# Performance work log

Measured on AMD Instinct MI355X. Metric: run time of the kernel, lower is better.

Reference implementation:

```python
import jax, jax.numpy as jnp
import numpy as np

N_EMBED = 512  # c in the original; scale uses sqrt(c), not head_size


def setup_inputs() -> dict:
    key = jax.random.key(0)
    k1, k2, k3, k4 = jax.random.split(key, 4)
    B, T, C, H = 4, 4096, N_EMBED, 64
    x = jax.random.normal(k1, (B, T, C), dtype=jnp.float32)
    Wk = jax.random.normal(k2, (C, H), dtype=jnp.float32) * (1.0 / np.sqrt(C))
    Wq = jax.random.normal(k3, (C, H), dtype=jnp.float32) * (1.0 / np.sqrt(C))
    Wv = jax.random.normal(k4, (C, H), dtype=jnp.float32) * (1.0 / np.sqrt(C))
    return {"x": x, "Wk": Wk, "Wq": Wq, "Wv": Wv}


def reference(x, Wk, Wq, Wv):
    # x: [B, T, C]; Wk/Wq/Wv: [C, H]
    B, T, C = x.shape
    k = jnp.einsum('btc,ch->bth', x, Wk)
    q = jnp.einsum('btc,ch->bth', x, Wq)
    v = jnp.einsum('btc,ch->bth', x, Wv)
    scale = 1.0 / jnp.sqrt(jnp.float32(C))  # original divides by sqrt(c)
    scores = jnp.einsum('bth,bsh->bts', q, k) * scale  # [B, T, T]
    causal = jnp.tril(jnp.ones((T, T), dtype=bool))
    scores = jnp.where(causal, scores, -jnp.inf)
    attn = jax.nn.softmax(scores, axis=-1)
    # dropout = 0.0 -> identity
    out = jnp.einsum('bts,bsh->bth', attn, v)  # [B, T, H]
    return out
```

## Files before the change

kernel.cpp:

```cpp
#include <hip/hip_runtime.h>
#include <hip/hip_bf16.h>
#include <math.h>

#define NB 4
#define NT 4096
#define NC 512
#define NH 64
#define QBLK 64
#define KVBLK 64
#define LDK 72
#define MASKV (-1e30f)

typedef __attribute__((ext_vector_type(8))) short bf16x8;
typedef __attribute__((ext_vector_type(4))) float f32x4;

__device__ inline unsigned short f2bf(float f) {
    __hip_bfloat16 h = __float2bfloat16(f);
    return *reinterpret_cast<unsigned short*>(&h);
}

__device__ inline int part_slot(int b, int qt, int ch) {
    int m = qt >> 3, r = qt & 7;
    return b * 288 + qt + 4 * m * (m - 1) + r * m + ch;
}

__global__ __launch_bounds__(256) void wconv(
    const float* __restrict__ Wk, const float* __restrict__ Wq,
    const float* __restrict__ Wv, unsigned short* __restrict__ Wt)
{
    int idx = blockIdx.x * 256 + threadIdx.x;
    int n = idx % 192, c = idx / 192;
    int sel = n >> 6, h = n & 63;
    const float* W = (sel == 0) ? Wq : (sel == 1) ? Wk : Wv;
    float val = W[c * NH + h];
    if (sel == 0) val *= 0.044194173824159216f;
    Wt[n * NC + c] = f2bf(val);
}

__global__ __launch_bounds__(256) void qkv_gemm(
    const float* __restrict__ x, const unsigned short* __restrict__ Wt,
    unsigned short* __restrict__ q, unsigned short* __restrict__ k,
    unsigned short* __restrict__ v)
{
    __shared__ unsigned short xa[32][LDK];
    __shared__ unsigned short wb[192][LDK];

    const int tid = threadIdx.x;
    const int w = tid >> 6, lane = tid & 63, l15 = lane & 15, g = lane >> 4;
    const size_t r0 = (size_t)blockIdx.x * 32;

    f32x4 acc[2][3];
    #pragma unroll
    for (int mt = 0; mt < 2; ++mt)
        #pragma unroll
        for (int nt = 0; nt < 3; ++nt) acc[mt][nt] = (f32x4){0.f,0.f,0.f,0.f};

    for (int c0 = 0; c0 < NC; c0 += 64) {
        __syncthreads();
        {
            int row = tid >> 3, f8 = tid & 7;
            const float* xp = x + (r0 + row) * NC + c0 + f8*8;
            float4 x0 = *reinterpret_cast<const float4*>(xp);
            float4 x1 = *reinterpret_cast<const float4*>(xp + 4);
            bf16x8 a8;
            a8[0]=f2bf(x0.x); a8[1]=f2bf(x0.y); a8[2]=f2bf(x0.z); a8[3]=f2bf(x0.w);
            a8[4]=f2bf(x1.x); a8[5]=f2bf(x1.y); a8[6]=f2bf(x1.z); a8[7]=f2bf(x1.w);
            *reinterpret_cast<bf16x8*>(&xa[row][f8*8]) = a8;
        }
        #pragma unroll
        for (int i = 0; i < 6; ++i) {
            int idx = tid + 256*i;
            int row = idx >> 3, f8 = idx & 7;
            bf16x8 w8 = *reinterpret_cast<const bf16x8*>(Wt + (size_t)row * NC + c0 + f8*8);
            *reinterpret_cast<bf16x8*>(&wb[row][f8*8]) = w8;
        }
        __syncthreads();

        #pragma unroll
        for (int kk = 0; kk < 2; ++kk) {
            bf16x8 a[2], bfr[3];
            #pragma unroll
            for (int mt = 0; mt < 2; ++mt)
                a[mt] = *reinterpret_cast<const bf16x8*>(&xa[16*mt + l15][32*kk + 8*g]);
            #pragma unroll
            for (int nt = 0; nt < 3; ++nt)
                bfr[nt] = *reinterpret_cast<const bf16x8*>(&wb[48*w + 16*nt + l15][32*kk + 8*g]);
            __builtin_amdgcn_s_setprio(1);
            #pragma unroll
            for (int mt = 0; mt < 2; ++mt)
                #pragma unroll
                for (int nt = 0; nt < 3; ++nt)
                    acc[mt][nt] = __builtin_amdgcn_mfma_f32_16x16x32_bf16(a[mt], bfr[nt], acc[mt][nt], 0, 0, 0);
            __builtin_amdgcn_s_setprio(0);
        }
    }

    #pragma unroll
    for (int mt = 0; mt < 2; ++mt)
        #pragma unroll
        for (int nt = 0; nt < 3; ++nt) {
            int ncol = 48*w + 16*nt + l15;
            int sel = ncol >> 6, h = ncol & 63;
            unsigned short* dst = (sel == 0) ? q : (sel == 1) ? k : v;
            #pragma unroll
            for (int r = 0; r < 4; ++r)
                dst[(r0 + 16*mt + 4*g + r) * NH + h] = f2bf(acc[mt][nt][r]);
        }
}

__global__ __launch_bounds__(256) void attn_part(
    const unsigned short* __restrict__ qg,
    const unsigned short* __restrict__ kg,
    const unsigned short* __restrict__ vg,
    float* __restrict__ out,
    float* __restrict__ O_part,
    float* __restrict__ ML_part)
{
    const int qt = 63 - blockIdx.x;
    const int ch = blockIdx.y;
    if (8*ch > qt) return;
    const int b  = blockIdx.z;
    const int nch = (qt >> 3) + 1;

    __shared__ unsigned short k_lds[2][KVBLK][LDK];
    __shared__ unsigned short vt_lds[2][NH][LDK];
    __shared__ unsigned short p_lds[4][16][LDK];

    const int tid  = threadIdx.x;
    const int w    = tid >> 6;
    const int lane = tid & 63;
    const int l15  = lane & 15;
    const int g    = lane >> 4;

    const int q0 = qt * QBLK;
    const size_t base = (size_t)b * NT * NH;
    const int qrow  = q0 + 16*w + l15;
    const int wrow0 = q0 + 16*w;
    const int qhi   = wrow0 + 15;

    bf16x8 qf0, qf1;
    {
        const unsigned short* qp = qg + base + (size_t)qrow * NH + 8*g;
        qf0 = *reinterpret_cast<const bf16x8*>(qp);
        qf1 = *reinterpret_cast<const bf16x8*>(qp + 32);
    }

    f32x4 ot[4];
    #pragma unroll
    for (int i = 0; i < 4; ++i) ot[i] = (f32x4){0.f,0.f,0.f,0.f};
    float m = MASKV, lsum = 0.f;

    const int tBeg = 8 * ch;
    const int tEnd = min(8 * (ch + 1), qt + 1);

    const int krow = tid >> 3, kc8 = tid & 7;
    const int vd = lane, vkq = w;

    bf16x8 kpre0, kpre1;
    unsigned short vpre[16];

    {
        const int s0 = tBeg * KVBLK;
        const unsigned short* kp = kg + base + (size_t)(s0 + krow) * NH + kc8*8;
        kpre0 = *reinterpret_cast<const bf16x8*>(kp);
        kpre1 = *reinterpret_cast<const bf16x8*>(kp + 32 * NH);
        #pragma unroll
        for (int i = 0; i < 16; ++i)
            vpre[i] = vg[base + (size_t)(s0 + vkq*16 + i) * NH + vd];
    }

    int cur = 0;
    for (int it = tBeg; it < tEnd; ++it) {
        const int s0 = it * KVBLK;
        *reinterpret_cast<bf16x8*>(&k_lds[cur][krow][kc8*8])      = kpre0;
        *reinterpret_cast<bf16x8*>(&k_lds[cur][krow+32][kc8*8])   = kpre1;
        *reinterpret_cast<bf16x8*>(&vt_lds[cur][vd][vkq*16])      = *reinterpret_cast<bf16x8*>(&vpre[0]);
        *reinterpret_cast<bf16x8*>(&vt_lds[cur][vd][vkq*16 + 8])  = *reinterpret_cast<bf16x8*>(&vpre[8]);
        __syncthreads();

        if (it + 1 < tEnd) {
            const int sn = s0 + KVBLK;
            const unsigned short* kp = kg + base + (size_t)(sn + krow) * NH + kc8*8;
            kpre0 = *reinterpret_cast<const bf16x8*>(kp);
            kpre1 = *reinterpret_cast<const bf16x8*>(kp + 32 * NH);
            #pragma unroll
            for (int i = 0; i < 16; ++i)
                vpre[i] = vg[base + (size_t)(sn + vkq*16 + i) * NH + vd];
        }

        if (s0 <= qhi) {
            f32x4 s[4];
            __builtin_amdgcn_s_setprio(1);
            #pragma unroll
            for (int t = 0; t < 4; ++t) {
                bf16x8 ka = *reinterpret_cast<const bf16x8*>(&k_lds[cur][16*t + l15][8*g]);
                bf16x8 kb = *reinterpret_cast<const bf16x8*>(&k_lds[cur][16*t + l15][8*g + 32]);
                s[t] = __builtin_amdgcn_mfma_f32_16x16x32_bf16(ka, qf0, (f32x4){0.f,0.f,0.f,0.f}, 0, 0, 0);
                s[t] = __builtin_amdgcn_mfma_f32_16x16x32_bf16(kb, qf1, s[t], 0, 0, 0);
            }
            __builtin_amdgcn_s_setprio(0);

            if (s0 + 63 > wrow0) {
                const int kvb = s0 + 4*g;
                #pragma unroll
                for (int t = 0; t < 4; ++t)
                    #pragma unroll
                    for (int r = 0; r < 4; ++r)
                        if (kvb + 16*t + r > qrow) s[t][r] = MASKV;
            }

            float pm = MASKV;
            #pragma unroll
            for (int t = 0; t < 4; ++t)
                #pragma unroll
                for (int r = 0; r < 4; ++r) pm = fmaxf(pm, s[t][r]);
            pm = fmaxf(pm, __shfl_xor(pm, 16));
            pm = fmaxf(pm, __shfl_xor(pm, 32));

            if (!__all(pm <= m + 8.f)) {
                float mn   = fmaxf(m, pm);
                float corr = __expf(m - mn);
                lsum *= corr;
                #pragma unroll
                for (int dt = 0; dt < 4; ++dt)
                    #pragma unroll
                    for (int e = 0; e < 4; ++e) ot[dt][e] *= corr;
                m = mn;
            }

            float ps = 0.f;
            #pragma unroll
            for (int t = 0; t < 4; ++t)
                #pragma unroll
                for (int r = 0; r < 4; ++r) {
                    float pv = __expf(s[t][r] - m);
                    s[t][r] = pv;
                    ps += pv;
                }

            #pragma unroll
            for (int t = 0; t < 4; ++t) {
                unsigned int w0 = (unsigned int)f2bf(s[t][0]) | ((unsigned int)f2bf(s[t][1]) << 16);
                unsigned int w1 = (unsigned int)f2bf(s[t][2]) | ((unsigned int)f2bf(s[t][3]) << 16);
                *reinterpret_cast<unsigned int*>(&p_lds[w][l15][16*t + 4*g])     = w0;
                *reinterpret_cast<unsigned int*>(&p_lds[w][l15][16*t + 4*g + 2]) = w1;
            }

            ps += __shfl_xor(ps, 16);
            ps += __shfl_xor(ps, 32);
            lsum += ps;

            __builtin_amdgcn_s_setprio(1);
            #pragma unroll
            for (int kk = 0; kk < 2; ++kk) {
                bf16x8 pf = *reinterpret_cast<const bf16x8*>(&p_lds[w][l15][8*g + 32*kk]);
                #pragma unroll
                for (int dt = 0; dt < 4; ++dt) {
                    bf16x8 vf = *reinterpret_cast<const bf16x8*>(&vt_lds[cur][16*dt + l15][8*g + 32*kk]);
                    ot[dt] = __builtin_amdgcn_mfma_f32_16x16x32_bf16(vf, pf, ot[dt], 0, 0, 0);
                }
            }
            __builtin_amdgcn_s_setprio(0);
        }
        cur ^= 1;
    }

    if (nch == 1) {
        const float inv = 1.f / lsum;
        float* orow = out + base + (size_t)qrow * NH;
        #pragma unroll
        for (int dt = 0; dt < 4; ++dt) {
            f32x4 o4;
            #pragma unroll
            for (int r = 0; r < 4; ++r) o4[r] = ot[dt][r] * inv;
            *reinterpret_cast<f32x4*>(&orow[16*dt + 4*g]) = o4;
        }
    } else {
        const int slot = part_slot(b, qt, ch);
        float* op = O_part + (size_t)slot * (QBLK*NH) + (size_t)(16*w + l15) * NH;
        #pragma unroll
        for (int dt = 0; dt < 4; ++dt)
            *reinterpret_cast<f32x4*>(&op[16*dt + 4*g]) = ot[dt];
        if (g == 0) {
            float2 ml = make_float2(m, lsum);
            *reinterpret_cast<float2*>(&ML_part[(size_t)slot * 128 + 2*(16*w + l15)]) = ml;
        }
    }
}

__global__ __launch_bounds__(256) void attn_merge(
    const float* __restrict__ O_part,
    const float* __restrict__ ML_part,
    float* __restrict__ out)
{
    const int qt = 8 + blockIdx.x;
    const int b  = blockIdx.y;
    const int nch = (qt >> 3) + 1;
    const int slot0 = part_slot(b, qt, 0);
    const int row = threadIdx.x >> 2;
    const int dq  = (threadIdx.x & 3) * 16;

    float M = MASKV;
    #pragma unroll 2
    for (int c = 0; c < nch; ++c)
        M = fmaxf(M, ML_part[(size_t)(slot0 + c) * 128 + 2*row]);

    float L = 0.f;
    float acc[16];
    #pragma unroll
    for (int j = 0; j < 16; ++j) acc[j] = 0.f;

    for (int c = 0; c < nch; ++c) {
        const float* mlp = &ML_part[(size_t)(slot0 + c) * 128 + 2*row];
        float mc = mlp[0], lc = mlp[1];
        float wgt = __expf(mc - M);
        L += wgt * lc;
        const float* op = O_part + (size_t)(slot0 + c) * (QBLK*NH) + (size_t)row * NH + dq;
        #pragma unroll
        for (int j4 = 0; j4 < 4; ++j4) {
            float4 o4 = *reinterpret_cast<const float4*>(op + 4*j4);
            acc[4*j4+0] = fmaf(wgt, o4.x, acc[4*j4+0]);
            acc[4*j4+1] = fmaf(wgt, o4.y, acc[4*j4+1]);
            acc[4*j4+2] = fmaf(wgt, o4.z, acc[4*j4+2]);
            acc[4*j4+3] = fmaf(wgt, o4.w, acc[4*j4+3]);
        }
    }

    const float inv = 1.f / L;
    float* orow = out + (size_t)b * NT * NH + (size_t)(qt * QBLK + row) * NH + dq;
    #pragma unroll
    for (int j4 = 0; j4 < 4; ++j4) {
        float4 o4;
        o4.x = acc[4*j4+0] * inv;
        o4.y = acc[4*j4+1] * inv;
        o4.z = acc[4*j4+2] * inv;
        o4.w = acc[4*j4+3] * inv;
        *reinterpret_cast<float4*>(orow + 4*j4) = o4;
    }
}

extern "C" void kernel_launch(void* const* d_in, const int* in_sizes, int n_in,
                              void* d_out, int out_size, void* d_ws, size_t ws_size,
                              hipStream_t stream) {
    const float* x  = (const float*)d_in[0];
    const float* Wk = (const float*)d_in[1];
    const float* Wq = (const float*)d_in[2];
    const float* Wv = (const float*)d_in[3];
    float* out = (float*)d_out;

    const size_t n = (size_t)NB * NT * NH;
    unsigned short* qb = (unsigned short*)d_ws;
    unsigned short* kb = qb + n;
    unsigned short* vb = kb + n;
    unsigned short* Wt = vb + n;
    float* O_part  = (float*)(Wt + 192 * NC);
    float* ML_part = O_part + (size_t)1152 * QBLK * NH;

    wconv<<<(192*NC)/256, 256, 0, stream>>>(Wk, Wq, Wv, Wt);
    qkv_gemm<<<(NB*NT)/32, 256, 0, stream>>>(x, Wt, qb, kb, vb);

    dim3 pgrid(64, 8, NB);
    attn_part<<<pgrid, 256, 0, stream>>>(qb, kb, vb, out, O_part, ML_part);
    dim3 mgrid(56, NB);
    attn_merge<<<mgrid, 256, 0, stream>>>(O_part, ML_part, out);
}
```

Baseline: 64.94 us.

## Restructure attention into single-wave 32-row blocks reading K and transposed V directly

The QKV GEMM now writes V already transposed to [B,H,T], so the attention kernel can load V fragments straight from global memory. The attention kernel becomes a one-wave block handling 32 query rows (two 16-row MFMA tiles) with no K/V staging in shared memory and no block barriers, which raises the block count and removes sync and LDS traffic. The split-KV partition and merge indexing are redone for 32-row tiles. The cost is more global/L2 reads, since each wave fetches its own K/V tiles, and a larger partial-result buffer.

```diff
diff --git a/kernel.cpp b/kernel.cpp
--- a/kernel.cpp
+++ b/kernel.cpp
@@ -6,7 +6,6 @@
 #define NT 4096
 #define NC 512
 #define NH 64
-#define QBLK 64
 #define KVBLK 64
 #define LDK 72
 #define MASKV (-1e30f)
@@ -17,11 +16,6 @@
 __device__ inline unsigned short f2bf(float f) {
     __hip_bfloat16 h = __float2bfloat16(f);
     return *reinterpret_cast<unsigned short*>(&h);
-}
-
-__device__ inline int part_slot(int b, int qt, int ch) {
-    int m = qt >> 3, r = qt & 7;
-    return b * 288 + qt + 4 * m * (m - 1) + r * m + ch;
 }
 
 __global__ __launch_bounds__(256) void wconv(
@@ -40,7 +34,7 @@
 __global__ __launch_bounds__(256) void qkv_gemm(
     const float* __restrict__ x, const unsigned short* __restrict__ Wt,
     unsigned short* __restrict__ q, unsigned short* __restrict__ k,
-    unsigned short* __restrict__ v)
+    unsigned short* __restrict__ vt)
 {
     __shared__ unsigned short xa[32][LDK];
     __shared__ unsigned short wb[192][LDK];
@@ -101,189 +95,197 @@
         for (int nt = 0; nt < 3; ++nt) {
             int ncol = 48*w + 16*nt + l15;
             int sel = ncol >> 6, h = ncol & 63;
-            unsigned short* dst = (sel == 0) ? q : (sel == 1) ? k : v;
-            #pragma unroll
-            for (int r = 0; r < 4; ++r)
-                dst[(r0 + 16*mt + 4*g + r) * NH + h] = f2bf(acc[mt][nt][r]);
-        }
-}
-
-__global__ __launch_bounds__(256) void attn_part(
+            if (sel < 2) {
+                unsigned short* dst = (sel == 0) ? q : k;
+                #pragma unroll
+                for (int r = 0; r < 4; ++r)
+                    dst[(r0 + 16*mt + 4*g + r) * NH + h] = f2bf(acc[mt][nt][r]);
+            } else {
+                int bb = (int)(r0 >> 12);
+                int trow = ((int)r0 & (NT-1)) + 16*mt + 4*g;
+                unsigned int lo = (unsigned int)f2bf(acc[mt][nt][0]) | ((unsigned int)f2bf(acc[mt][nt][1]) << 16);
+                unsigned int hi = (unsigned int)f2bf(acc[mt][nt][2]) | ((unsigned int)f2bf(acc[mt][nt][3]) << 16);
+                *reinterpret_cast<uint2*>(&vt[((size_t)bb*NH + h)*NT + trow]) = make_uint2(lo, hi);
+            }
+        }
+}
+
+__global__ __launch_bounds__(64, 3) void attn_part(
     const unsigned short* __restrict__ qg,
     const unsigned short* __restrict__ kg,
-    const unsigned short* __restrict__ vg,
+    const unsigned short* __restrict__ vtg,
     float* __restrict__ out,
     float* __restrict__ O_part,
     float* __restrict__ ML_part)
 {
-    const int qt = 63 - blockIdx.x;
+    const int qt = 127 - blockIdx.x;
+    const int nT = (qt >> 1) + 1;
     const int ch = blockIdx.y;
-    if (8*ch > qt) return;
+    if (8 * ch >= nT) return;
     const int b  = blockIdx.z;
-    const int nch = (qt >> 3) + 1;
-
-    __shared__ unsigned short k_lds[2][KVBLK][LDK];
-    __shared__ unsigned short vt_lds[2][NH][LDK];
-    __shared__ unsigned short p_lds[4][16][LDK];
-
-    const int tid  = threadIdx.x;
-    const int w    = tid >> 6;
-    const int lane = tid & 63;
+
+    __shared__ unsigned short p_lds[32][LDK];
+
+    const int lane = threadIdx.x & 63;
     const int l15  = lane & 15;
     const int g    = lane >> 4;
 
-    const int q0 = qt * QBLK;
+    const int q0 = qt * 32;
     const size_t base = (size_t)b * NT * NH;
-    const int qrow  = q0 + 16*w + l15;
-    const int wrow0 = q0 + 16*w;
-    const int qhi   = wrow0 + 15;
-
-    bf16x8 qf0, qf1;
-    {
-        const unsigned short* qp = qg + base + (size_t)qrow * NH + 8*g;
-        qf0 = *reinterpret_cast<const bf16x8*>(qp);
-        qf1 = *reinterpret_cast<const bf16x8*>(qp + 32);
-    }
-
-    f32x4 ot[4];
-    #pragma unroll
-    for (int i = 0; i < 4; ++i) ot[i] = (f32x4){0.f,0.f,0.f,0.f};
-    float m = MASKV, lsum = 0.f;
+
+    bf16x8 qf[2][2];
+    #pragma unroll
+    for (int qc = 0; qc < 2; ++qc) {
+        const unsigned short* qp = qg + base + (size_t)(q0 + 16*qc + l15) * NH + 8*g;
+        qf[qc][0] = *reinterpret_cast<const bf16x8*>(qp);
+        qf[qc][1] = *reinterpret_cast<const bf16x8*>(qp + 32);
+    }
+
+    f32x4 ot[4][2];
+    #pragma unroll
+    for (int dt = 0; dt < 4; ++dt)
+        #pragma unroll
+        for (int qc = 0; qc < 2; ++qc) ot[dt][qc] = (f32x4){0.f,0.f,0.f,0.f};
+    float m0 = MASKV, m1 = MASKV, l0 = 0.f, l1 = 0.f;
 
     const int tBeg = 8 * ch;
-    const int tEnd = min(8 * (ch + 1), qt + 1);
-
-    const int krow = tid >> 3, kc8 = tid & 7;
-    const int vd = lane, vkq = w;
-
-    bf16x8 kpre0, kpre1;
-    unsigned short vpre[16];
-
-    {
-        const int s0 = tBeg * KVBLK;
-        const unsigned short* kp = kg + base + (size_t)(s0 + krow) * NH + kc8*8;
-        kpre0 = *reinterpret_cast<const bf16x8*>(kp);
-        kpre1 = *reinterpret_cast<const bf16x8*>(kp + 32 * NH);
-        #pragma unroll
-        for (int i = 0; i < 16; ++i)
-            vpre[i] = vg[base + (size_t)(s0 + vkq*16 + i) * NH + vd];
-    }
-
-    int cur = 0;
+    const int tEnd = min(8 * (ch + 1), nT);
+
     for (int it = tBeg; it < tEnd; ++it) {
         const int s0 = it * KVBLK;
-        *reinterpret_cast<bf16x8*>(&k_lds[cur][krow][kc8*8])      = kpre0;
-        *reinterpret_cast<bf16x8*>(&k_lds[cur][krow+32][kc8*8])   = kpre1;
-        *reinterpret_cast<bf16x8*>(&vt_lds[cur][vd][vkq*16])      = *reinterpret_cast<bf16x8*>(&vpre[0]);
-        *reinterpret_cast<bf16x8*>(&vt_lds[cur][vd][vkq*16 + 8])  = *reinterpret_cast<bf16x8*>(&vpre[8]);
-        __syncthreads();
-
-        if (it + 1 < tEnd) {
-            const int sn = s0 + KVBLK;
-            const unsigned short* kp = kg + base + (size_t)(sn + krow) * NH + kc8*8;
-            kpre0 = *reinterpret_cast<const bf16x8*>(kp);
-            kpre1 = *reinterpret_cast<const bf16x8*>(kp + 32 * NH);
-            #pragma unroll
-            for (int i = 0; i < 16; ++i)
-                vpre[i] = vg[base + (size_t)(sn + vkq*16 + i) * NH + vd];
-        }
-
-        if (s0 <= qhi) {
-            f32x4 s[4];
-            __builtin_amdgcn_s_setprio(1);
-            #pragma unroll
-            for (int t = 0; t < 4; ++t) {
-                bf16x8 ka = *reinterpret_cast<const bf16x8*>(&k_lds[cur][16*t + l15][8*g]);
-                bf16x8 kb = *reinterpret_cast<const bf16x8*>(&k_lds[cur][16*t + l15][8*g + 32]);
-                s[t] = __builtin_amdgcn_mfma_f32_16x16x32_bf16(ka, qf0, (f32x4){0.f,0.f,0.f,0.f}, 0, 0, 0);
-                s[t] = __builtin_amdgcn_mfma_f32_16x16x32_bf16(kb, qf1, s[t], 0, 0, 0);
-            }
-            __builtin_amdgcn_s_setprio(0);
-
-            if (s0 + 63 > wrow0) {
-                const int kvb = s0 + 4*g;
-                #pragma unroll
-                for (int t = 0; t < 4; ++t)
+
+        const unsigned short* kbase = kg + base + (size_t)(s0 + l15) * NH + 8*g;
+        bf16x8 ka[4][2];
+        #pragma unroll
+        for (int t = 0; t < 4; ++t)
+            #pragma unroll
+            for (int kk = 0; kk < 2; ++kk)
+                ka[t][kk] = *reinterpret_cast<const bf16x8*>(kbase + t*16*NH + kk*32);
+
+        f32x4 s[4][2];
+        __builtin_amdgcn_s_setprio(1);
+        #pragma unroll
+        for (int t = 0; t < 4; ++t)
+            #pragma unroll
+            for (int qc = 0; qc < 2; ++qc) {
+                s[t][qc] = __builtin_amdgcn_mfma_f32_16x16x32_bf16(ka[t][0], qf[qc][0], (f32x4){0.f,0.f,0.f,0.f}, 0, 0, 0);
+                s[t][qc] = __builtin_amdgcn_mfma_f32_16x16x32_bf16(ka[t][1], qf[qc][1], s[t][qc], 0, 0, 0);
+            }
+        __builtin_amdgcn_s_setprio(0);
+
+        const unsigned short* vbase = vtg + ((size_t)b*NH + l15)*NT + s0 + 8*g;
+        bf16x8 vf[4][2];
+        #pragma unroll
+        for (int dt = 0; dt < 4; ++dt)
+            #pragma unroll
+            for (int kk = 0; kk < 2; ++kk)
+                vf[dt][kk] = *reinterpret_cast<const bf16x8*>(vbase + (size_t)dt*16*NT + kk*32);
+
+        if (s0 + KVBLK - 1 > q0) {
+            #pragma unroll
+            for (int t = 0; t < 4; ++t)
+                #pragma unroll
+                for (int qc = 0; qc < 2; ++qc) {
+                    const int qr = q0 + 16*qc + l15;
                     #pragma unroll
                     for (int r = 0; r < 4; ++r)
-                        if (kvb + 16*t + r > qrow) s[t][r] = MASKV;
-            }
-
-            float pm = MASKV;
-            #pragma unroll
-            for (int t = 0; t < 4; ++t)
-                #pragma unroll
-                for (int r = 0; r < 4; ++r) pm = fmaxf(pm, s[t][r]);
-            pm = fmaxf(pm, __shfl_xor(pm, 16));
-            pm = fmaxf(pm, __shfl_xor(pm, 32));
-
-            if (!__all(pm <= m + 8.f)) {
-                float mn   = fmaxf(m, pm);
-                float corr = __expf(m - mn);
-                lsum *= corr;
-                #pragma unroll
-                for (int dt = 0; dt < 4; ++dt)
-                    #pragma unroll
-                    for (int e = 0; e < 4; ++e) ot[dt][e] *= corr;
-                m = mn;
-            }
-
-            float ps = 0.f;
-            #pragma unroll
-            for (int t = 0; t < 4; ++t)
-                #pragma unroll
-                for (int r = 0; r < 4; ++r) {
-                    float pv = __expf(s[t][r] - m);
-                    s[t][r] = pv;
-                    ps += pv;
+                        if (s0 + 16*t + 4*g + r > qr) s[t][qc][r] = MASKV;
                 }
-
+        }
+
+        float pm0 = MASKV, pm1 = MASKV;
+        #pragma unroll
+        for (int t = 0; t < 4; ++t)
+            #pragma unroll
+            for (int r = 0; r < 4; ++r) {
+                pm0 = fmaxf(pm0, s[t][0][r]);
+                pm1 = fmaxf(pm1, s[t][1][r]);
+            }
+        pm0 = fmaxf(pm0, __shfl_xor(pm0, 16)); pm0 = fmaxf(pm0, __shfl_xor(pm0, 32));
+        pm1 = fmaxf(pm1, __shfl_xor(pm1, 16)); pm1 = fmaxf(pm1, __shfl_xor(pm1, 32));
+
+        if (!__all(pm0 <= m0 + 8.f && pm1 <= m1 + 8.f)) {
+            float mn0 = fmaxf(m0, pm0), mn1 = fmaxf(m1, pm1);
+            float c0 = __expf(m0 - mn0), c1 = __expf(m1 - mn1);
+            l0 *= c0; l1 *= c1;
+            #pragma unroll
+            for (int dt = 0; dt < 4; ++dt)
+                #pragma unroll
+                for (int e = 0; e < 4; ++e) {
+                    ot[dt][0][e] *= c0;
+                    ot[dt][1][e] *= c1;
+                }
+            m0 = mn0; m1 = mn1;
+        }
+
+        float ps0 = 0.f, ps1 = 0.f;
+        #pragma unroll
+        for (int t = 0; t < 4; ++t)
+            #pragma unroll
+            for (int r = 0; r < 4; ++r) {
+                float p0 = __expf(s[t][0][r] - m0);
+                float p1 = __expf(s[t][1][r] - m1);
+                s[t][0][r] = p0; s[t][1][r] = p1;
+                ps0 += p0; ps1 += p1;
+            }
+
+        #pragma unroll
+        for (int qc = 0; qc < 2; ++qc)
             #pragma unroll
             for (int t = 0; t < 4; ++t) {
-                unsigned int w0 = (unsigned int)f2bf(s[t][0]) | ((unsigned int)f2bf(s[t][1]) << 16);
-                unsigned int w1 = (unsigned int)f2bf(s[t][2]) | ((unsigned int)f2bf(s[t][3]) << 16);
-                *reinterpret_cast<unsigned int*>(&p_lds[w][l15][16*t + 4*g])     = w0;
-                *reinterpret_cast<unsigned int*>(&p_lds[w][l15][16*t + 4*g + 2]) = w1;
-            }
-
-            ps += __shfl_xor(ps, 16);
-            ps += __shfl_xor(ps, 32);
-            lsum += ps;
-
-            __builtin_amdgcn_s_setprio(1);
-            #pragma unroll
-            for (int kk = 0; kk < 2; ++kk) {
-                bf16x8 pf = *reinterpret_cast<const bf16x8*>(&p_lds[w][l15][8*g + 32*kk]);
-                #pragma unroll
-                for (int dt = 0; dt < 4; ++dt) {
-                    bf16x8 vf = *reinterpret_cast<const bf16x8*>(&vt_lds[cur][16*dt + l15][8*g + 32*kk]);
-                    ot[dt] = __builtin_amdgcn_mfma_f32_16x16x32_bf16(vf, pf, ot[dt], 0, 0, 0);
-                }
-            }
-            __builtin_amdgcn_s_setprio(0);
-        }
-        cur ^= 1;
-    }
-
-    if (nch == 1) {
-        const float inv = 1.f / lsum;
-        float* orow = out + base + (size_t)qrow * NH;
-        #pragma unroll
-        for (int dt = 0; dt < 4; ++dt) {
-            f32x4 o4;
-            #pragma unroll
-            for (int r = 0; r < 4; ++r) o4[r] = ot[dt][r] * inv;
-            *reinterpret_cast<f32x4*>(&orow[16*dt + 4*g]) = o4;
+                unsigned int w0 = (unsigned int)f2bf(s[t][qc][0]) | ((unsigned int)f2bf(s[t][qc][1]) << 16);
+                unsigned int w1 = (unsigned int)f2bf(s[t][qc][2]) | ((unsigned int)f2bf(s[t][qc][3]) << 16);
+                *reinterpret_cast<unsigned int*>(&p_lds[16*qc + l15][16*t + 4*g])     = w0;
+                *reinterpret_cast<unsigned int*>(&p_lds[16*qc + l15][16*t + 4*g + 2]) = w1;
+            }
+
+        ps0 += __shfl_xor(ps0, 16); ps0 += __shfl_xor(ps0, 32);
+        ps1 += __shfl_xor(ps1, 16); ps1 += __shfl_xor(ps1, 32);
+        l0 += ps0; l1 += ps1;
+
+        bf16x8 pf[2][2];
+        #pragma unroll
+        for (int qc = 0; qc < 2; ++qc)
+            #pragma unroll
+            for (int kk = 0; kk < 2; ++kk)
+                pf[qc][kk] = *reinterpret_cast<const bf16x8*>(&p_lds[16*qc + l15][8*g + 32*kk]);
+        __builtin_amdgcn_s_setprio(1);
+        #pragma unroll
+        for (int kk = 0; kk < 2; ++kk)
+            #pragma unroll
+            for (int dt = 0; dt < 4; ++dt)
+                #pragma unroll
+                for (int qc = 0; qc < 2; ++qc)
+                    ot[dt][qc] = __builtin_amdgcn_mfma_f32_16x16x32_bf16(vf[dt][kk], pf[qc][kk], ot[dt][qc], 0, 0, 0);
+        __builtin_amdgcn_s_setprio(0);
+    }
+
+    if (nT <= 8) {
+        const float inv0 = 1.f / l0, inv1 = 1.f / l1;
+        #pragma unroll
+        for (int qc = 0; qc < 2; ++qc) {
+            float inv = qc ? inv1 : inv0;
+            float* orow = out + base + (size_t)(q0 + 16*qc + l15) * NH;
+            #pragma unroll
+            for (int dt = 0; dt < 4; ++dt) {
+                f32x4 o4;
+                #pragma unroll
+                for (int r = 0; r < 4; ++r) o4[r] = ot[dt][qc][r] * inv;
+                *reinterpret_cast<f32x4*>(&orow[16*dt + 4*g]) = o4;
+            }
         }
     } else {
-        const int slot = part_slot(b, qt, ch);
-        float* op = O_part + (size_t)slot * (QBLK*NH) + (size_t)(16*w + l15) * NH;
-        #pragma unroll
-        for (int dt = 0; dt < 4; ++dt)
-            *reinterpret_cast<f32x4*>(&op[16*dt + 4*g]) = ot[dt];
+        const int slot = ((b * 128 + qt) << 3) + ch;
+        float* op = O_part + (size_t)slot * (32*NH);
+        #pragma unroll
+        for (int qc = 0; qc < 2; ++qc)
+            #pragma unroll
+            for (int dt = 0; dt < 4; ++dt)
+                *reinterpret_cast<f32x4*>(&op[(size_t)(16*qc + l15) * NH + 16*dt + 4*g]) = ot[dt][qc];
         if (g == 0) {
-            float2 ml = make_float2(m, lsum);
-            *reinterpret_cast<float2*>(&ML_part[(size_t)slot * 128 + 2*(16*w + l15)]) = ml;
+            float* mlp = ML_part + (size_t)slot * 64;
+            *reinterpret_cast<float2*>(&mlp[2*l15])        = make_float2(m0, l0);
+            *reinterpret_cast<float2*>(&mlp[2*(16 + l15)]) = make_float2(m1, l1);
         }
     }
 }
@@ -293,31 +295,29 @@
     const float* __restrict__ ML_part,
     float* __restrict__ out)
 {
-    const int qt = 8 + blockIdx.x;
+    const int qt = 16 + blockIdx.x;
     const int b  = blockIdx.y;
-    const int nch = (qt >> 3) + 1;
-    const int slot0 = part_slot(b, qt, 0);
-    const int row = threadIdx.x >> 2;
-    const int dq  = (threadIdx.x & 3) * 16;
+    const int nch = (((qt >> 1) + 1) + 7) >> 3;
+    const int slot0 = ((b * 128 + qt) << 3);
+    const int row = threadIdx.x >> 3;
+    const int dq  = (threadIdx.x & 7) * 8;
 
     float M = MASKV;
-    #pragma unroll 2
     for (int c = 0; c < nch; ++c)
-        M = fmaxf(M, ML_part[(size_t)(slot0 + c) * 128 + 2*row]);
+        M = fmaxf(M, ML_part[(size_t)(slot0 + c) * 64 + 2*row]);
 
     float L = 0.f;
-    float acc[16];
-    #pragma unroll
-    for (int j = 0; j < 16; ++j) acc[j] = 0.f;
+    float acc[8];
+    #pragma unroll
+    for (int j = 0; j < 8; ++j) acc[j] = 0.f;
 
     for (int c = 0; c < nch; ++c) {
-        const float* mlp = &ML_part[(size_t)(slot0 + c) * 128 + 2*row];
-        float mc = mlp[0], lc = mlp[1];
-        float wgt = __expf(mc - M);
-        L += wgt * lc;
-        const float* op = O_part + (size_t)(slot0 + c) * (QBLK*NH) + (size_t)row * NH + dq;
-        #pragma unroll
-        for (int j4 = 0; j4 < 4; ++j4) {
+        const float* mlp = &ML_part[(size_t)(slot0 + c) * 64 + 2*row];
+        float wgt = __expf(mlp[0] - M);
+        L += wgt * mlp[1];
+        const float* op = O_part + (size_t)(slot0 + c) * (32*NH) + (size_t)row * NH + dq;
+        #pragma unroll
+        for (int j4 = 0; j4 < 2; ++j4) {
             float4 o4 = *reinterpret_cast<const float4*>(op + 4*j4);
             acc[4*j4+0] = fmaf(wgt, o4.x, acc[4*j4+0]);
             acc[4*j4+1] = fmaf(wgt, o4.y, acc[4*j4+1]);
@@ -327,9 +327,9 @@
     }
 
     const float inv = 1.f / L;
-    float* orow = out + (size_t)b * NT * NH + (size_t)(qt * QBLK + row) * NH + dq;
-    #pragma unroll
-    for (int j4 = 0; j4 < 4; ++j4) {
+    float* orow = out + (size_t)b * NT * NH + (size_t)(qt * 32 + row) * NH + dq;
+    #pragma unroll
+    for (int j4 = 0; j4 < 2; ++j4) {
         float4 o4;
         o4.x = acc[4*j4+0] * inv;
         o4.y = acc[4*j4+1] * inv;
@@ -351,16 +351,16 @@
     const size_t n = (size_t)NB * NT * NH;
     unsigned short* qb = (unsigned short*)d_ws;
     unsigned short* kb = qb + n;
-    unsigned short* vb = kb + n;
-    unsigned short* Wt = vb + n;
+    unsigned short* vt = kb + n;
+    unsigned short* Wt = vt + n;
     float* O_part  = (float*)(Wt + 192 * NC);
-    float* ML_part = O_part + (size_t)1152 * QBLK * NH;
+    float* ML_part = O_part + (size_t)4096 * 32 * NH;
 
     wconv<<<(192*NC)/256, 256, 0, stream>>>(Wk, Wq, Wv, Wt);
-    qkv_gemm<<<(NB*NT)/32, 256, 0, stream>>>(x, Wt, qb, kb, vb);
-
-    dim3 pgrid(64, 8, NB);
-    attn_part<<<pgrid, 256, 0, stream>>>(qb, kb, vb, out, O_part, ML_part);
-    dim3 mgrid(56, NB);
+    qkv_gemm<<<(NB*NT)/32, 256, 0, stream>>>(x, Wt, qb, kb, vt);
+
+    dim3 pgrid(128, 8, NB);
+    attn_part<<<pgrid, 64, 0, stream>>>(qb, kb, vt, out, O_part, ML_part);
+    dim3 mgrid(112, NB);
     attn_merge<<<mgrid, 256, 0, stream>>>(O_part, ML_part, out);
 }
```

Measured after the change: 73.76 us. 13.6% more time.
